# Optimization experiments

Measured on AMD Instinct MI355X. Metric: run time of the kernel, lower is better.

Reference implementation:

```python
import jax, jax.numpy as jnp
import numpy as np

B, T, DQ, DF, H, D = 64, 4096, 512, 256, 8, 64
EPS = 1e-7

def setup_inputs() -> dict:
    key = jax.random.key(0)
    ks = jax.random.split(key, 6)
    return {
        "query": jax.random.normal(ks[0], (B, 1, DQ), dtype=jnp.float32),
        "fact": jax.random.normal(ks[1], (B, T, DF), dtype=jnp.float32),
        "Wq": jax.random.normal(ks[2], (H, DQ, D), dtype=jnp.float32) / np.sqrt(DQ).astype(np.float32),
        "bq": jax.random.normal(ks[3], (H, D), dtype=jnp.float32) * 0.1,
        "Wf": jax.random.normal(ks[4], (H, DF, D), dtype=jnp.float32) / np.sqrt(DF).astype(np.float32),
        "bf": jax.random.normal(ks[5], (H, D), dtype=jnp.float32) * 0.1,
    }

def reference(query, fact, Wq, bq, Wf, bf):
    # Per-head linear projections, batched over the head axis h.
    # fc_query: [B, H, 1, D]; fc_fact: [B, H, T, D]
    fq = jnp.einsum('bqf,hfd->bhqd', query, Wq) + bq[None, :, None, :]
    ff = jnp.einsum('btf,hfd->bhtd', fact, Wf) + bf[None, :, None, :]
    # dot = fc_fact @ fc_query^T -> [B, H, T, 1]
    dot = jnp.einsum('bhtd,bhqd->bhtq', ff, fq)
    # softmax over the sequence (torch dim=1 of [B, T, 1]) + epsilon
    alphas = jax.nn.softmax(dot, axis=2) + EPS
    # out_k = fc_fact^T @ alphas -> [B, H, D, 1]; concat heads on dim 1, squeeze dim 2
    out = jnp.einsum('bhtd,bhtq->bhdq', ff, alphas)
    return out.reshape(out.shape[0], H * D)
```

## Files before the change

### kernel.cpp

```cpp
#include <hip/hip_runtime.h>
#include <hip/hip_bf16.h>

#define B_ 64
#define T_ 4096
#define DQ_ 512
#define DF_ 256
#define H_ 8
#define D_ 64
#define EPS_ 1e-7f
#define NBLK 512
#define CHUNK 32
#define NCH 16
#define PS_STRIDE 2304
#define ROWB 1040
#define SLOTS 2080
#define BUFB (SLOTS * 16)

typedef __attribute__((ext_vector_type(8))) short short8;
typedef __attribute__((ext_vector_type(4))) float f32x4;

union U8 { uint4 u; short8 s; };

#if defined(__has_builtin)
#if __has_builtin(__builtin_amdgcn_global_load_lds)
#define HAVE_GLL 1
#endif
#endif

#ifdef HAVE_GLL
static __device__ __forceinline__ void STAGE16(const void* g, void* l) {
  __builtin_amdgcn_global_load_lds(
      (const __attribute__((address_space(1))) unsigned int*)g,
      (__attribute__((address_space(3))) unsigned int*)l, 16, 0, 0);
}
#else
static __device__ __forceinline__ void STAGE16(const void* g, void* l) {
  *(float4*)l = *(const float4*)g;
}
#endif

static __device__ __forceinline__ unsigned int pk2(float a, float b) {
  __hip_bfloat162 h = __float22bfloat162_rn(make_float2(a, b));
  union { __hip_bfloat162 h; unsigned int u; } c; c.h = h;
  return c.u;
}

__global__ __launch_bounds__(256) void prep_fq(const float* __restrict__ qin,
    const float* __restrict__ Wq, const float* __restrict__ bq,
    float* __restrict__ fq) {
  __shared__ float qs[DQ_];
  __shared__ float red[4][D_];
  int bh = blockIdx.x, b = bh >> 3, h = bh & 7;
  int tid = threadIdx.x, d = tid & 63, fc = tid >> 6;
  qs[tid] = qin[(size_t)b * DQ_ + tid];
  qs[tid + 256] = qin[(size_t)b * DQ_ + tid + 256];
  __syncthreads();
  const float* w = Wq + (size_t)h * DQ_ * D_ + (size_t)fc * 128 * D_ + d;
  float acc = 0.f;
#pragma unroll 8
  for (int i = 0; i < 128; ++i) acc += qs[fc * 128 + i] * w[(size_t)i * D_];
  red[fc][d] = acc;
  __syncthreads();
  if (fc == 0)
    fq[(size_t)bh * D_ + d] = acc + red[1][d] + red[2][d] + red[3][d] + bq[h * D_ + d];
}

__global__ __launch_bounds__(256) void prep_v(const float* __restrict__ Wf,
    const float* __restrict__ fq, unsigned short* __restrict__ vB) {
  __shared__ float fql[D_];
  int bh = blockIdx.x, b = bh >> 3, h = bh & 7;
  int k = threadIdx.x;
  if (k < D_) fql[k] = fq[(size_t)bh * D_ + k];
  __syncthreads();
  const float4* wr = (const float4*)(Wf + (size_t)h * DF_ * D_ + (size_t)k * D_);
  const float4* f4 = (const float4*)fql;
  float acc = 0.f;
#pragma unroll
  for (int i = 0; i < 16; ++i) {
    float4 wv = wr[i], fv = f4[i];
    acc += wv.x * fv.x + wv.y * fv.y + wv.z * fv.z + wv.w * fv.w;
  }
  int ks = k >> 5, kg = (k >> 3) & 3, j = k & 7;
  size_t base = (size_t)b * 4096 + ks * 512;
  vB[base + (kg * 16 + h) * 8 + j] = (unsigned short)(pk2(acc, 0.f) & 0xFFFF);
  vB[base + (kg * 16 + 8 + h) * 8 + j] = 0;
}

__global__ __launch_bounds__(256, 2) void mha_main(
    const float* __restrict__ fact, const unsigned short* __restrict__ vB,
    float* __restrict__ part_s, float* __restrict__ part_ml) {
  __shared__ char buf[2 * BUFB];
  __shared__ float4 exch[2][4][64];

  const int tid = threadIdx.x;
  const int l = tid & 63, w = tid >> 6;
  const int dl = l & 15, kg = l >> 4;
  const int bid = blockIdx.x;
  const int b = bid >> 3, qq = bid & 7;

  short8 vfrag[2];
#pragma unroll
  for (int ks = 0; ks < 2; ++ks)
    vfrag[ks] = *(const short8*)(vB + (size_t)b * 4096 + (2 * w + ks) * 512 + l * 8);

  const float* factb = fact + ((size_t)b * T_ + (size_t)qq * 512) * DF_;

  int srow[9], sslot[9];
#pragma unroll
  for (int i = 0; i < 9; ++i) {
    int id = i * 256 + tid;
    srow[i] = id / 65;
    sslot[i] = id % 65;
  }

#define ISSUE(C) {                                                            \
    const char* gsrc = (const char*)(factb + (size_t)(C) * CHUNK * DF_);      \
    char* ldst = buf + ((C) & 1) * BUFB;                                      \
    _Pragma("unroll") for (int i = 0; i < 9; ++i) {                           \
      int id = i * 256 + tid;                                                 \
      if (i < 8 || id < SLOTS) {                                              \
        const void* sp = (sslot[i] < 64)                                      \
            ? (const void*)(gsrc + (size_t)srow[i] * 1024 + sslot[i] * 16)    \
            : (const void*)gsrc;                                              \
        STAGE16(sp, (void*)(ldst + id * 16));                                 \
      } } }

  float m_run = -INFINITY, l_part = 0.f;
  f32x4 acc_s[4];
#pragma unroll
  for (int n = 0; n < 4; ++n) { f32x4 z = {0.f, 0.f, 0.f, 0.f}; acc_s[n] = z; }

  ISSUE(0);

  for (int c = 0; c < NCH; ++c) {
    __syncthreads();
    if (c + 1 < NCH) ISSUE(c + 1);
    const char* bc = buf + (c & 1) * BUFB;

    f32x4 dp[2];
#pragma unroll
    for (int t2 = 0; t2 < 2; ++t2) {
      const char* arow = bc + (t2 * 16 + dl) * ROWB + (w * 64 + kg * 8) * 4;
      float4 a0 = *(const float4*)arow;
      float4 a1 = *(const float4*)(arow + 16);
      float4 a2 = *(const float4*)(arow + 128);
      float4 a3 = *(const float4*)(arow + 144);
      U8 af0, af1;
      af0.u.x = pk2(a0.x, a0.y); af0.u.y = pk2(a0.z, a0.w);
      af0.u.z = pk2(a1.x, a1.y); af0.u.w = pk2(a1.z, a1.w);
      af1.u.x = pk2(a2.x, a2.y); af1.u.y = pk2(a2.z, a2.w);
      af1.u.z = pk2(a3.x, a3.y); af1.u.w = pk2(a3.z, a3.w);
      f32x4 d_ = {0.f, 0.f, 0.f, 0.f};
      d_ = __builtin_amdgcn_mfma_f32_16x16x32_bf16(af0.s, vfrag[0], d_, 0, 0, 0);
      d_ = __builtin_amdgcn_mfma_f32_16x16x32_bf16(af1.s, vfrag[1], d_, 0, 0, 0);
      dp[t2] = d_;
      exch[t2][w][l] = make_float4(d_[0], d_[1], d_[2], d_[3]);
    }
    __syncthreads();

    f32x4 l0 = dp[0], l1 = dp[1];
#pragma unroll
    for (int ww = 1; ww < 4; ++ww) {
      int o = (w + ww) & 3;
      float4 p0 = exch[0][o][l], p1 = exch[1][o][l];
      l0[0] += p0.x; l0[1] += p0.y; l0[2] += p0.z; l0[3] += p0.w;
      l1[0] += p1.x; l1[1] += p1.y; l1[2] += p1.z; l1[3] += p1.w;
    }

    float tmax = fmaxf(fmaxf(fmaxf(l0[0], l0[1]), fmaxf(l0[2], l0[3])),
                       fmaxf(fmaxf(l1[0], l1[1]), fmaxf(l1[2], l1[3])));
    tmax = fmaxf(tmax, __shfl_xor(tmax, 16));
    tmax = fmaxf(tmax, __shfl_xor(tmax, 32));
    int need = (tmax > m_run + 8.f) && (dl < 8);
    if (__any(need)) {
      float mnew = fmaxf(m_run, tmax);
      float f = __expf(m_run - mnew);
      m_run = mnew;
      l_part *= f;
      float f0 = __shfl(f, kg * 4 + 0), f1 = __shfl(f, kg * 4 + 1);
      float f2 = __shfl(f, kg * 4 + 2), f3 = __shfl(f, kg * 4 + 3);
      if (kg < 2) {
#pragma unroll
        for (int n = 0; n < 4; ++n) {
          acc_s[n][0] *= f0; acc_s[n][1] *= f1; acc_s[n][2] *= f2; acc_s[n][3] *= f3;
        }
      }
    }
    float e0 = __expf(l0[0] - m_run), e1 = __expf(l0[1] - m_run);
    float e2 = __expf(l0[2] - m_run), e3 = __expf(l0[3] - m_run);
    float e4 = __expf(l1[0] - m_run), e5 = __expf(l1[1] - m_run);
    float e6 = __expf(l1[2] - m_run), e7 = __expf(l1[3] - m_run);
    l_part += (e0 + e1 + e2 + e3) + (e4 + e5 + e6 + e7);

    unsigned int pk00 = pk2(e0, e1), pk01 = pk2(e2, e3);
    unsigned int pk10 = pk2(e4, e5), pk11 = pk2(e6, e7);
    if (dl == 8) { pk00 = pk01 = pk10 = pk11 = 0x3F803F80u; }

    int sa = dl + ((kg & 1) ? 32 : 0);
    int sb = sa + 16;
    unsigned int g00 = __shfl(pk00, sa), g01 = __shfl(pk01, sa);
    unsigned int g02 = __shfl(pk00, sb), g03 = __shfl(pk01, sb);
    unsigned int g10 = __shfl(pk10, sa), g11 = __shfl(pk11, sa);
    unsigned int g12 = __shfl(pk10, sb), g13 = __shfl(pk11, sb);
    U8 eA;
    eA.u.x = (kg < 2) ? g00 : g10;
    eA.u.y = (kg < 2) ? g01 : g11;
    eA.u.z = (kg < 2) ? g02 : g12;
    eA.u.w = (kg < 2) ? g03 : g13;

#pragma unroll
    for (int n = 0; n < 4; ++n) {
      const char* srd = bc + (w * 64 + n * 16 + dl) * 4;
      float b0 = *(const float*)(srd + (kg * 8 + 0) * ROWB);
      float b1 = *(const float*)(srd + (kg * 8 + 1) * ROWB);
      float b2 = *(const float*)(srd + (kg * 8 + 2) * ROWB);
      float b3 = *(const float*)(srd + (kg * 8 + 3) * ROWB);
      float b4 = *(const float*)(srd + (kg * 8 + 4) * ROWB);
      float b5 = *(const float*)(srd + (kg * 8 + 5) * ROWB);
      float b6 = *(const float*)(srd + (kg * 8 + 6) * ROWB);
      float b7 = *(const float*)(srd + (kg * 8 + 7) * ROWB);
      U8 bb;
      bb.u.x = pk2(b0, b1); bb.u.y = pk2(b2, b3);
      bb.u.z = pk2(b4, b5); bb.u.w = pk2(b6, b7);
      acc_s[n] = __builtin_amdgcn_mfma_f32_16x16x32_bf16(eA.s, bb.s, acc_s[n], 0, 0, 0);
    }
  }

  l_part += __shfl_xor(l_part, 16);
  l_part += __shfl_xor(l_part, 32);
  if (w == 0 && l < 8) {
    part_ml[(size_t)bid * 16 + l] = m_run;
    part_ml[(size_t)bid * 16 + 8 + l] = l_part;
  }
  float* ps = part_s + (size_t)bid * PS_STRIDE;
  if (kg < 2) {
#pragma unroll
    for (int n = 0; n < 4; ++n) {
      int f = w * 64 + n * 16 + dl;
      ps[(kg * 4 + 0) * 256 + f] = acc_s[n][0];
      ps[(kg * 4 + 1) * 256 + f] = acc_s[n][1];
      ps[(kg * 4 + 2) * 256 + f] = acc_s[n][2];
      ps[(kg * 4 + 3) * 256 + f] = acc_s[n][3];
    }
  } else if (kg == 2) {
#pragma unroll
    for (int n = 0; n < 4; ++n)
      ps[8 * 256 + w * 64 + n * 16 + dl] = acc_s[n][0];
  }
}

__global__ __launch_bounds__(64) void reduce_k(const float* __restrict__ part_s,
    const float* __restrict__ part_ml, const float* __restrict__ Wf,
    const float* __restrict__ bf, float* __restrict__ out) {
  __shared__ float s_l[DF_];
  int bh = blockIdx.x, b = bh >> 3, h = bh & 7;
  int d = threadIdx.x;
  float M = -INFINITY;
  float mq[8];
#pragma unroll
  for (int q = 0; q < 8; ++q) {
    mq[q] = part_ml[(size_t)(b * 8 + q) * 16 + h];
    M = fmaxf(M, mq[q]);
  }
  float L = 0.f;
  float sa[4] = {0.f, 0.f, 0.f, 0.f}, cs[4] = {0.f, 0.f, 0.f, 0.f};
#pragma unroll
  for (int q = 0; q < 8; ++q) {
    float e = __expf(mq[q] - M);
    L += e * part_ml[(size_t)(b * 8 + q) * 16 + 8 + h];
    const float* ps = part_s + (size_t)(b * 8 + q) * PS_STRIDE;
#pragma unroll
    for (int c = 0; c < 4; ++c) {
      sa[c] += e * ps[h * 256 + c * 64 + d];
      cs[c] += ps[8 * 256 + c * 64 + d];
    }
  }
  float inv = 1.f / L;
#pragma unroll
  for (int c = 0; c < 4; ++c) s_l[c * 64 + d] = sa[c] * inv + EPS_ * cs[c];
  __syncthreads();
  const float* wcol = Wf + (size_t)h * DF_ * D_ + d;
  float o = 0.f;
#pragma unroll 8
  for (int k = 0; k < DF_; ++k) o += s_l[k] * wcol[(size_t)k * D_];
  o += (1.f + (float)T_ * EPS_) * bf[h * D_ + d];
  out[(size_t)b * (H_ * D_) + h * D_ + d] = o;
}

extern "C" void kernel_launch(void* const* d_in, const int* in_sizes, int n_in,
                              void* d_out, int out_size, void* d_ws, size_t ws_size,
                              hipStream_t stream) {
  const float* query = (const float*)d_in[0];
  const float* fact  = (const float*)d_in[1];
  const float* Wq    = (const float*)d_in[2];
  const float* bq    = (const float*)d_in[3];
  const float* Wf    = (const float*)d_in[4];
  const float* bf    = (const float*)d_in[5];
  float* out = (float*)d_out;

  char* ws = (char*)d_ws;
  float* fq = (float*)ws;
  unsigned short* vB = (unsigned short*)(ws + 131072);
  float* part_ml = (float*)(ws + 655360);
  float* part_s = (float*)(ws + 688128);

  prep_fq<<<dim3(B_ * H_), dim3(256), 0, stream>>>(query, Wq, bq, fq);
  prep_v<<<dim3(B_ * H_), dim3(256), 0, stream>>>(Wf, fq, vB);
  mha_main<<<dim3(NBLK), dim3(256), 0, stream>>>(fact, vB, part_s, part_ml);
  reduce_k<<<dim3(B_ * H_), dim3(64), 0, stream>>>(part_s, part_ml, Wf, bf, out);
}
```

Baseline: 83.78 us.

## Fuse prep kernels, swizzle LDS rows, move prefetch after barrier, widen reduce

Merges the two prep kernels into one, which removes a launch and the global round-trip for fq. Adds an XOR-like row rotation by kg to the staged fact layout so the column-strided B-operand LDS reads avoid bank conflicts. Moves the next-chunk prefetch after the second barrier, and widens reduce_k to 256 threads with a split-K partial sum so it has more parallelism. The swizzle has to match exactly between the staging writes and both read paths, otherwise results are wrong.

```diff
diff --git a/kernel.cpp b/kernel.cpp
--- a/kernel.cpp
+++ b/kernel.cpp
@@ -45,34 +45,29 @@
   return c.u;
 }
 
-__global__ __launch_bounds__(256) void prep_fq(const float* __restrict__ qin,
+__global__ __launch_bounds__(256) void prep(const float* __restrict__ qin,
     const float* __restrict__ Wq, const float* __restrict__ bq,
-    float* __restrict__ fq) {
+    const float* __restrict__ Wf, unsigned short* __restrict__ vB) {
   __shared__ float qs[DQ_];
   __shared__ float red[4][D_];
+  __shared__ float fql[D_];
   int bh = blockIdx.x, b = bh >> 3, h = bh & 7;
   int tid = threadIdx.x, d = tid & 63, fc = tid >> 6;
   qs[tid] = qin[(size_t)b * DQ_ + tid];
   qs[tid + 256] = qin[(size_t)b * DQ_ + tid + 256];
   __syncthreads();
-  const float* w = Wq + (size_t)h * DQ_ * D_ + (size_t)fc * 128 * D_ + d;
-  float acc = 0.f;
+  {
+    const float* w = Wq + (size_t)h * DQ_ * D_ + (size_t)fc * 128 * D_ + d;
+    float acc = 0.f;
 #pragma unroll 8
-  for (int i = 0; i < 128; ++i) acc += qs[fc * 128 + i] * w[(size_t)i * D_];
-  red[fc][d] = acc;
+    for (int i = 0; i < 128; ++i) acc += qs[fc * 128 + i] * w[(size_t)i * D_];
+    red[fc][d] = acc;
+  }
   __syncthreads();
   if (fc == 0)
-    fq[(size_t)bh * D_ + d] = acc + red[1][d] + red[2][d] + red[3][d] + bq[h * D_ + d];
-}
-
-__global__ __launch_bounds__(256) void prep_v(const float* __restrict__ Wf,
-    const float* __restrict__ fq, unsigned short* __restrict__ vB) {
-  __shared__ float fql[D_];
-  int bh = blockIdx.x, b = bh >> 3, h = bh & 7;
-  int k = threadIdx.x;
-  if (k < D_) fql[k] = fq[(size_t)bh * D_ + k];
-  __syncthreads();
-  const float4* wr = (const float4*)(Wf + (size_t)h * DF_ * D_ + (size_t)k * D_);
+    fql[d] = red[0][d] + red[1][d] + red[2][d] + red[3][d] + bq[h * D_ + d];
+  __syncthreads();
+  const float4* wr = (const float4*)(Wf + (size_t)h * DF_ * D_ + (size_t)tid * D_);
   const float4* f4 = (const float4*)fql;
   float acc = 0.f;
 #pragma unroll
@@ -80,7 +75,7 @@
     float4 wv = wr[i], fv = f4[i];
     acc += wv.x * fv.x + wv.y * fv.y + wv.z * fv.z + wv.w * fv.w;
   }
-  int ks = k >> 5, kg = (k >> 3) & 3, j = k & 7;
+  int ks = tid >> 5, kg = (tid >> 3) & 3, j = tid & 7;
   size_t base = (size_t)b * 4096 + ks * 512;
   vB[base + (kg * 16 + h) * 8 + j] = (unsigned short)(pk2(acc, 0.f) & 0xFFFF);
   vB[base + (kg * 16 + 8 + h) * 8 + j] = 0;
@@ -109,9 +104,21 @@
 #pragma unroll
   for (int i = 0; i < 9; ++i) {
     int id = i * 256 + tid;
-    srow[i] = id / 65;
+    int rho = id / 65;
+    int kgr = (rho >> 3) & 3;
+    srow[i] = (rho & ~7) | (((rho & 7) + 8 - 2 * kgr) & 7);
     sslot[i] = id % 65;
   }
+
+  const int t0 = dl, t1 = 16 + dl;
+  const int lr0 = (t0 & ~7) | (((t0 & 7) + 2 * ((t0 >> 3) & 3)) & 7);
+  const int lr1 = (t1 & ~7) | (((t1 & 7) + 2 * ((t1 >> 3) & 3)) & 7);
+  const int aoff0 = lr0 * ROWB + (w * 64 + kg * 8) * 4;
+  const int aoff1 = lr1 * ROWB + (w * 64 + kg * 8) * 4;
+  int roff[8];
+#pragma unroll
+  for (int j = 0; j < 8; ++j)
+    roff[j] = (kg * 8 + ((j + 2 * kg) & 7)) * ROWB;
 
 #define ISSUE(C) {                                                            \
     const char* gsrc = (const char*)(factb + (size_t)(C) * CHUNK * DF_);      \
@@ -134,13 +141,12 @@
 
   for (int c = 0; c < NCH; ++c) {
     __syncthreads();
-    if (c + 1 < NCH) ISSUE(c + 1);
     const char* bc = buf + (c & 1) * BUFB;
 
     f32x4 dp[2];
 #pragma unroll
     for (int t2 = 0; t2 < 2; ++t2) {
-      const char* arow = bc + (t2 * 16 + dl) * ROWB + (w * 64 + kg * 8) * 4;
+      const char* arow = bc + (t2 ? aoff1 : aoff0);
       float4 a0 = *(const float4*)arow;
       float4 a1 = *(const float4*)(arow + 16);
       float4 a2 = *(const float4*)(arow + 128);
@@ -158,6 +164,8 @@
     }
     __syncthreads();
 
+    if (c + 1 < NCH) ISSUE(c + 1);
+
     f32x4 l0 = dp[0], l1 = dp[1];
 #pragma unroll
     for (int ww = 1; ww < 4; ++ww) {
@@ -210,15 +218,15 @@
 
 #pragma unroll
     for (int n = 0; n < 4; ++n) {
-      const char* srd = bc + (w * 64 + n * 16 + dl) * 4;
-      float b0 = *(const float*)(srd + (kg * 8 + 0) * ROWB);
-      float b1 = *(const float*)(srd + (kg * 8 + 1) * ROWB);
-      float b2 = *(const float*)(srd + (kg * 8 + 2) * ROWB);
-      float b3 = *(const float*)(srd + (kg * 8 + 3) * ROWB);
-      float b4 = *(const float*)(srd + (kg * 8 + 4) * ROWB);
-      float b5 = *(const float*)(srd + (kg * 8 + 5) * ROWB);
-      float b6 = *(const float*)(srd + (kg * 8 + 6) * ROWB);
-      float b7 = *(const float*)(srd + (kg * 8 + 7) * ROWB);
+      const char* srd = bc + (size_t)(w * 64 + n * 16 + dl) * 4;
+      float b0 = *(const float*)(srd + roff[0]);
+      float b1 = *(const float*)(srd + roff[1]);
+      float b2 = *(const float*)(srd + roff[2]);
+      float b3 = *(const float*)(srd + roff[3]);
+      float b4 = *(const float*)(srd + roff[4]);
+      float b5 = *(const float*)(srd + roff[5]);
+      float b6 = *(const float*)(srd + roff[6]);
+      float b7 = *(const float*)(srd + roff[7]);
       U8 bb;
       bb.u.x = pk2(b0, b1); bb.u.y = pk2(b2, b3);
       bb.u.z = pk2(b4, b5); bb.u.w = pk2(b6, b7);
@@ -249,12 +257,13 @@
   }
 }
 
-__global__ __launch_bounds__(64) void reduce_k(const float* __restrict__ part_s,
+__global__ __launch_bounds__(256) void reduce_k(const float* __restrict__ part_s,
     const float* __restrict__ part_ml, const float* __restrict__ Wf,
     const float* __restrict__ bf, float* __restrict__ out) {
   __shared__ float s_l[DF_];
+  __shared__ float red[4][D_];
   int bh = blockIdx.x, b = bh >> 3, h = bh & 7;
-  int d = threadIdx.x;
+  int tid = threadIdx.x, d = tid & 63, fc = tid >> 6;
   float M = -INFINITY;
   float mq[8];
 #pragma unroll
@@ -262,29 +271,26 @@
     mq[q] = part_ml[(size_t)(b * 8 + q) * 16 + h];
     M = fmaxf(M, mq[q]);
   }
-  float L = 0.f;
-  float sa[4] = {0.f, 0.f, 0.f, 0.f}, cs[4] = {0.f, 0.f, 0.f, 0.f};
+  float L = 0.f, sa = 0.f, cs = 0.f;
 #pragma unroll
   for (int q = 0; q < 8; ++q) {
     float e = __expf(mq[q] - M);
     L += e * part_ml[(size_t)(b * 8 + q) * 16 + 8 + h];
     const float* ps = part_s + (size_t)(b * 8 + q) * PS_STRIDE;
-#pragma unroll
-    for (int c = 0; c < 4; ++c) {
-      sa[c] += e * ps[h * 256 + c * 64 + d];
-      cs[c] += ps[8 * 256 + c * 64 + d];
-    }
-  }
-  float inv = 1.f / L;
-#pragma unroll
-  for (int c = 0; c < 4; ++c) s_l[c * 64 + d] = sa[c] * inv + EPS_ * cs[c];
-  __syncthreads();
-  const float* wcol = Wf + (size_t)h * DF_ * D_ + d;
+    sa += e * ps[h * 256 + tid];
+    cs += ps[8 * 256 + tid];
+  }
+  s_l[tid] = sa / L + EPS_ * cs;
+  __syncthreads();
+  const float* wbase = Wf + (size_t)h * DF_ * D_ + (size_t)fc * 64 * D_ + d;
   float o = 0.f;
 #pragma unroll 8
-  for (int k = 0; k < DF_; ++k) o += s_l[k] * wcol[(size_t)k * D_];
-  o += (1.f + (float)T_ * EPS_) * bf[h * D_ + d];
-  out[(size_t)b * (H_ * D_) + h * D_ + d] = o;
+  for (int k = 0; k < 64; ++k) o += s_l[fc * 64 + k] * wbase[(size_t)k * D_];
+  red[fc][d] = o;
+  __syncthreads();
+  if (fc == 0)
+    out[(size_t)b * (H_ * D_) + h * D_ + d] =
+        o + red[1][d] + red[2][d] + red[3][d] + (1.f + (float)T_ * EPS_) * bf[h * D_ + d];
 }
 
 extern "C" void kernel_launch(void* const* d_in, const int* in_sizes, int n_in,
@@ -299,13 +305,11 @@
   float* out = (float*)d_out;
 
   char* ws = (char*)d_ws;
-  float* fq = (float*)ws;
-  unsigned short* vB = (unsigned short*)(ws + 131072);
-  float* part_ml = (float*)(ws + 655360);
-  float* part_s = (float*)(ws + 688128);
-
-  prep_fq<<<dim3(B_ * H_), dim3(256), 0, stream>>>(query, Wq, bq, fq);
-  prep_v<<<dim3(B_ * H_), dim3(256), 0, stream>>>(Wf, fq, vB);
+  unsigned short* vB = (unsigned short*)ws;
+  float* part_ml = (float*)(ws + 524288);
+  float* part_s = (float*)(ws + 557056);
+
+  prep<<<dim3(B_ * H_), dim3(256), 0, stream>>>(query, Wq, bq, Wf, vB);
   mha_main<<<dim3(NBLK), dim3(256), 0, stream>>>(fact, vB, part_s, part_ml);
-  reduce_k<<<dim3(B_ * H_), dim3(64), 0, stream>>>(part_s, part_ml, Wf, bf, out);
-}
+  reduce_k<<<dim3(B_ * H_), dim3(256), 0, stream>>>(part_s, part_ml, Wf, bf, out);
+}
```

New measurement: 68.80 us, median of 2. 1.22x faster.
